# Optimization experiments

Measured on AMD Instinct MI355X. Metric: run time of the kernel, lower is better.

Reference implementation:

```python
import jax, jax.numpy as jnp
import numpy as np

N, H, HD = 512, 8, 128          # n_nodes, n_heads, h feature dim
M0, M1 = 256, 256               # mlp_units
NORM_CONST = 1.0


def setup_inputs() -> dict:
    key = jax.random.key(0)
    ks = jax.random.split(key, 16)
    def w(k, i, o, scale=1.0):
        return jax.random.normal(k, (i, o), jnp.float32) * (scale / np.sqrt(i))
    F = HD + H * H               # h_concat dim = 128 + 64 = 192
    EIN = H + 2 * F              # edge MLP input dim = 8 + 384 = 392
    return {
        "x": jax.random.normal(ks[0], (N, H, 3), jnp.float32),
        "h": jax.random.normal(ks[1], (N, HD), jnp.float32),
        # phi_e: MLP([256,256], silu, activate_final=True)
        "We0": w(ks[2], EIN, M0), "be0": jnp.zeros((M0,), jnp.float32),
        "We1": w(ks[3], M0, M1), "be1": jnp.zeros((M1,), jnp.float32),
        # phi_inf: Linear(1) + sigmoid
        "Winf": w(ks[4], M1, 1), "binf": jnp.zeros((1,), jnp.float32),
        # phi_x: MLP([256,256], silu, activate_final=True) -> Linear(n_heads) (variance-scaled small init)
        "Wx0": w(ks[5], M1, M0), "bx0": jnp.zeros((M0,), jnp.float32),
        "Wx1": w(ks[6], M0, M1), "bx1": jnp.zeros((M1,), jnp.float32),
        "Wxo": w(ks[7], M1, H, scale=0.03), "bxo": jnp.zeros((H,), jnp.float32),
        # phi_h: MLP([256,256], silu, activate_final=False)... note haiku MLP applies
        # activation between layers; final Linear(h_dim) appended in forward.
        "Wh0": w(ks[8], M1 + HD, M0), "bh0": jnp.zeros((M0,), jnp.float32),
        "Wh1": w(ks[9], M0, M1), "bh1": jnp.zeros((M1,), jnp.float32),
        "Who": w(ks[10], M1, HD), "bho": jnp.zeros((HD,), jnp.float32),
    }


def _forward(x, h, We0, be0, We1, be1, Winf, binf, Wx0, bx0, Wx1, bx1,
             Wxo, bxo, Wh0, bh0, Wh1, bh1, Who, bho):
    n, nh = x.shape[0], x.shape[1]
    silu = jax.nn.silu
    off = 1.0 - jnp.eye(n, dtype=x.dtype)                  # off-diagonal node mask
    # per-node head-pair squared distances -> [N, H*H] (diag naturally 0)
    dh = x[:, :, None, :] - x[:, None, :, :]               # [N,H,H,3]
    sqh = jnp.sum(dh * dh, axis=-1).reshape(n, nh * nh)
    hc = jnp.concatenate([h, sqh], axis=-1)                # [N, F]
    # all-pairs node diffs per head: dn[i,j,h] = x[j,h] - x[i,h]
    dn = x[None] - x[:, None]                              # [N,N,H,3]
    sqn = jnp.sum(dn * dn, axis=-1)                        # [N,N,H]
    F = hc.shape[-1]
    hc_j = jnp.broadcast_to(hc[None], (n, n, F))           # receiver-side: hc[j]
    hc_i = jnp.broadcast_to(hc[:, None], (n, n, F))        # sender-side: hc[i]
    edge_in = jnp.concatenate([sqn, hc_j, hc_i], axis=-1)  # [N,N,H+2F]
    # phi_e (activate_final=True), zero self-edges
    m = silu(silu(edge_in @ We0 + be0) @ We1 + be1) * off[:, :, None]
    # gate + message aggregation
    e = jax.nn.sigmoid(m @ Winf + binf)[..., 0] * off      # [N,N]
    m_i = jnp.einsum('ijd,ij->id', m, e)                   # [N,M1]
    # phi_x multi-head coordinate weights (tanh=False), zero self-edges
    px = (silu(silu(m @ Wx0 + bx0) @ Wx1 + bx1) @ Wxo + bxo) * off[:, :, None]
    # normalize_by_x_norm=True path
    norm = jnp.sqrt(sqn + 1e-8) + NORM_CONST               # [N,N,H]
    ndiff = (dn / norm[..., None]) * off[:, :, None, None]
    shift = jnp.einsum('ijhd,ijh->ihd', ndiff, px) / (n - 1)  # agg='mean'
    x_new = x + shift
    # phi_h with residual
    ph_in = jnp.concatenate([m_i, h], axis=-1)
    h_new = h + silu(silu(ph_in @ Wh0 + bh0) @ Wh1 + bh1) @ Who + bho
    return x_new, h_new


def reference(x, h, We0, be0, We1, be1, Winf, binf, Wx0, bx0, Wx1, bx1,
              Wxo, bxo, Wh0, bh0, Wh1, bh1, Who, bho):
    return _forward(x, h, We0, be0, We1, be1, Winf, binf, Wx0, bx0, Wx1, bx1,
                    Wxo, bxo, Wh0, bh0, Wh1, bh1, Who, bho)
```

## Files before the change

kernel.cpp:

```cpp
#include <hip/hip_runtime.h>
#include <math.h>

#define N_NODES 512
#define NH 8
#define HD 128
#define M 256
#define PITCH 264
#define JTILE 64
#define RPW 16

typedef __bf16 v8bf __attribute__((ext_vector_type(8)));
typedef float f32x4 __attribute__((ext_vector_type(4)));
typedef unsigned short us4v __attribute__((ext_vector_type(4)));

__device__ __forceinline__ float silu_f(float v) {
  return v * __builtin_amdgcn_rcpf(1.f + __expf(-v));
}
__device__ __forceinline__ float sigmoid_f(float v) {
  return __builtin_amdgcn_rcpf(1.f + __expf(-v));
}
__device__ __forceinline__ unsigned short f2bf(float f) {
  unsigned u = __float_as_uint(f);
  u += 0x7fffu + ((u >> 16) & 1u);
  return (unsigned short)(u >> 16);
}
__device__ __forceinline__ unsigned short f2bf_hi(float f) {
  return (unsigned short)((__float_as_uint(f) + 0x8000u) >> 16);
}
__device__ __forceinline__ float bf2f(unsigned short s) {
  return __uint_as_float(((unsigned)s) << 16);
}

__device__ __forceinline__ void gl2lds16(const unsigned short* g, unsigned short* l) {
  __builtin_amdgcn_global_load_lds(
      (const __attribute__((address_space(1))) unsigned int*)g,
      (__attribute__((address_space(3))) unsigned int*)l, 16, 0, 0);
}

__global__ __launch_bounds__(256) void k_pre(
    const float* __restrict__ x, const float* __restrict__ h,
    const float* __restrict__ We0, const float* __restrict__ be0,
    const float* __restrict__ We1, const float* __restrict__ Wx0,
    const float* __restrict__ Wx1, const float* __restrict__ Wxo,
    unsigned short* __restrict__ wsB,
    float* __restrict__ P, float* __restrict__ Q,
    float* __restrict__ mi, float* __restrict__ shift)
{
  const int t = threadIdx.x;
  if (blockIdx.x < 816) {
    const int gid = blockIdx.x * 256 + t;
    if (gid >= 208896) return;
    float val;
    if (gid < 196608) {
      const int layer = gid >> 16;
      const int i2 = gid & 65535;
      const int j = i2 & 7, lane = (i2 >> 3) & 63, nt = (i2 >> 9) & 15, kt = i2 >> 13;
      const int k = kt * 32 + (lane >> 4) * 8 + j;
      const int n = nt * 16 + (lane & 15);
      const float* W = (layer == 0) ? We1 : (layer == 1) ? Wx0 : Wx1;
      val = W[k * 256 + n];
    } else if (gid < 200704) {
      const int i2 = gid - 196608;
      const int j = i2 & 7, lane = (i2 >> 3) & 63, kt = (i2 >> 9) & 7;
      const int k = kt * 32 + (lane >> 4) * 8 + j;
      const int n = lane & 15;
      val = (n < 8) ? Wxo[k * 8 + n] : 0.f;
    } else {
      const int i2 = gid - 200704;
      const int j = i2 & 7, lane = (i2 >> 3) & 63, nt = i2 >> 9;
      const int quad = lane >> 4, lnib = lane & 15;
      val = (quad == 0) ? We0[j * 256 + nt * 16 + lnib] : 0.f;
    }
    wsB[gid] = f2bf(val);
    return;
  }
  const int i = blockIdx.x - 816;
  __shared__ float s_x[24];
  __shared__ float s_hc[192];
  mi[i * M + t] = 0.f;
  if (t < 24) { shift[i * 24 + t] = 0.f; s_x[t] = x[i * 24 + t]; }
  __syncthreads();
  if (t < HD) {
    s_hc[t] = h[i * HD + t];
  } else if (t < 192) {
    const int p = t - HD, a = p >> 3, b = p & 7;
    float s = 0.f;
#pragma unroll
    for (int d = 0; d < 3; ++d) {
      const float dx = s_x[a * 3 + d] - s_x[b * 3 + d];
      s = fmaf(dx, dx, s);
    }
    s_hc[t] = s;
  }
  __syncthreads();
  float p = 0.f, q = 0.f;
  for (int k = 0; k < 192; ++k) {
    const float hv = s_hc[k];
    p = fmaf(hv, We0[(8 + k) * M + t], p);
    q = fmaf(hv, We0[(200 + k) * M + t], q);
  }
  P[i * M + t] = p;
  Q[i * M + t] = q + be0[t];
}

__global__ __launch_bounds__(512, 4) void k_edge(
    const float* __restrict__ x,
    const float* __restrict__ P, const float* __restrict__ Q,
    const float* __restrict__ be1,
    const float* __restrict__ Winf, const float* __restrict__ binf,
    const float* __restrict__ bx0, const float* __restrict__ bx1,
    const float* __restrict__ bxo,
    const unsigned short* __restrict__ wsB,
    float* __restrict__ mi_acc, float* __restrict__ shift_acc)
{
  const int i  = blockIdx.x;
  const int j0 = blockIdx.y * JTILE;
  const int t  = threadIdx.x;
  const int lane = t & 63, wave = t >> 6;
  const int lnib = lane & 15, quad = lane >> 4;
  const int rg = wave >> 1, c = wave & 1;
  const int r0 = rg * RPW;
  const int jw = j0 + r0;
  const int cb = c * 128;

  __shared__ __align__(16) unsigned short a_act[JTILE * PITCH];
  __shared__ __align__(16) unsigned short B_buf[8192];
  __shared__ __align__(16) float s_sqn[JTILE][8];
  __shared__ __align__(16) unsigned short s_sqnb[JTILE][8];
  __shared__ float s_red[JTILE][2];
  __shared__ float s_e[JTILE];

  auto stage = [&](const unsigned short* __restrict__ Bg, int kt) {
    const unsigned short* src = Bg + kt * 8192 + wave * 1024 + lane * 8;
    unsigned short* dst = &B_buf[wave * 1024];
    gl2lds16(src,       dst);
    gl2lds16(src + 512, dst + 512);
  };

#pragma unroll
  for (int kk = 0; kk < 2; ++kk) {
    const int idx = kk * 64 + lane;
    const int r = idx >> 3, hh = idx & 7;
    const int j = jw + r;
    float s = 0.f;
#pragma unroll
    for (int d = 0; d < 3; ++d) {
      const float dx = x[j * 24 + hh * 3 + d] - x[i * 24 + hh * 3 + d];
      s = fmaf(dx, dx, s);
    }
    s_sqn[r0 + r][hh] = s;
    s_sqnb[r0 + r][hh] = f2bf(s);
  }

  const float binf0 = binf[0];

  f32x4 acc[8];

  {
#pragma unroll
    for (int nt = 0; nt < 8; ++nt)
#pragma unroll
      for (int reg = 0; reg < 4; ++reg)
        acc[nt][reg] = P[(jw + quad * 4 + reg) * M + cb + nt * 16 + lnib];
    const v8bf aS = *(const v8bf*)&s_sqnb[r0 + lnib][0];
    const unsigned short* B0 = wsB + 200704;
#pragma unroll
    for (int nt = 0; nt < 8; ++nt) {
      const v8bf bv = *(const v8bf*)&B0[((c * 8 + nt) * 64 + lane) * 8];
      acc[nt] = __builtin_amdgcn_mfma_f32_16x16x32_bf16(aS, bv, acc[nt], 0, 0, 0);
    }
#pragma unroll
    for (int nt = 0; nt < 8; ++nt) {
      const float qv = Q[i * M + cb + nt * 16 + lnib];
#pragma unroll
      for (int reg = 0; reg < 4; ++reg) {
        const int row = r0 + quad * 4 + reg;
        a_act[row * PITCH + cb + nt * 16 + lnib] = f2bf_hi(silu_f(acc[nt][reg] + qv));
      }
    }
  }

  auto run_gemm = [&](const unsigned short* __restrict__ Bg) {
#pragma unroll
    for (int kt = 0; kt < 8; ++kt) {
      __syncthreads();
      stage(Bg, kt);
      __syncthreads();
      const v8bf a0 = *(const v8bf*)&a_act[(r0 + lnib) * PITCH + kt * 32 + quad * 8];
#pragma unroll
      for (int nt = 0; nt < 8; ++nt) {
        const v8bf bv = *(const v8bf*)&B_buf[(c * 8 + nt) * 512 + lane * 8];
        acc[nt] = __builtin_amdgcn_mfma_f32_16x16x32_bf16(a0, bv, acc[nt], 0, 0, 0);
      }
    }
    __syncthreads();
  };

#pragma unroll
  for (int nt = 0; nt < 8; ++nt) {
    const float b = be1[cb + nt * 16 + lnib];
    acc[nt] = (f32x4){b, b, b, b};
  }
  run_gemm(wsB);
  {
    float ge[4] = {0.f, 0.f, 0.f, 0.f};
#pragma unroll
    for (int nt = 0; nt < 8; ++nt) {
      const float wfv = Winf[cb + nt * 16 + lnib];
#pragma unroll
      for (int reg = 0; reg < 4; ++reg) {
        float v = silu_f(acc[nt][reg]);
        const int row = r0 + quad * 4 + reg;
        if (j0 + row == i) v = 0.f;
        a_act[row * PITCH + cb + nt * 16 + lnib] = f2bf_hi(v);
        ge[reg] = fmaf(v, wfv, ge[reg]);
      }
    }
#pragma unroll
    for (int reg = 0; reg < 4; ++reg) {
      float g = ge[reg];
      g += __shfl_xor(g, 1);
      g += __shfl_xor(g, 2);
      g += __shfl_xor(g, 4);
      g += __shfl_xor(g, 8);
      if (lnib == 0) s_red[r0 + quad * 4 + reg][c] = g;
    }
  }
  __syncthreads();
  if (t < JTILE) s_e[t] = sigmoid_f(s_red[t][0] + s_red[t][1] + binf0);
  __syncthreads();

  {
    const int ch = cb + lane * 2;
    float m0 = 0.f, m1 = 0.f;
#pragma unroll
    for (int r = 0; r < RPW; ++r) {
      const unsigned mv = *(const unsigned*)&a_act[(r0 + r) * PITCH + ch];
      const float ev = s_e[r0 + r];
      m0 = fmaf(bf2f((unsigned short)(mv & 0xffffu)), ev, m0);
      m1 = fmaf(bf2f((unsigned short)(mv >> 16)), ev, m1);
    }
    atomicAdd(&mi_acc[i * M + ch + 0], m0);
    atomicAdd(&mi_acc[i * M + ch + 1], m1);
  }

#pragma unroll
  for (int nt = 0; nt < 8; ++nt) {
    const float b = bx0[cb + nt * 16 + lnib];
    acc[nt] = (f32x4){b, b, b, b};
  }
  run_gemm(wsB + 65536);
#pragma unroll
  for (int nt = 0; nt < 8; ++nt)
#pragma unroll
    for (int reg = 0; reg < 4; ++reg) {
      const int row = r0 + quad * 4 + reg;
      a_act[row * PITCH + cb + nt * 16 + lnib] = f2bf_hi(silu_f(acc[nt][reg]));
    }

#pragma unroll
  for (int nt = 0; nt < 8; ++nt) {
    const float b = bx1[cb + nt * 16 + lnib];
    acc[nt] = (f32x4){b, b, b, b};
  }
  run_gemm(wsB + 131072);
#pragma unroll
  for (int nt = 0; nt < 8; ++nt)
#pragma unroll
    for (int reg = 0; reg < 4; ++reg) {
      const int row = r0 + quad * 4 + reg;
      a_act[row * PITCH + cb + nt * 16 + lnib] = f2bf_hi(silu_f(acc[nt][reg]));
    }
  __syncthreads();

  if (c == 0) {
    f32x4 px;
    {
      const float b = (lnib < 8) ? bxo[lnib] : 0.f;
      px = (f32x4){b, b, b, b};
      const unsigned short* B = wsB + 196608;
#pragma unroll
      for (int kt = 0; kt < 8; ++kt) {
        const v8bf a0 = *(const v8bf*)&a_act[(r0 + lnib) * PITCH + kt * 32 + quad * 8];
        const v8bf bv = *(const v8bf*)&B[(kt * 64 + lane) * 8];
        px = __builtin_amdgcn_mfma_f32_16x16x32_bf16(a0, bv, px, 0, 0, 0);
      }
    }
    const int hh = lnib & 7;
    const float xi0 = x[i * 24 + hh * 3 + 0];
    const float xi1 = x[i * 24 + hh * 3 + 1];
    const float xi2 = x[i * 24 + hh * 3 + 2];
    float p0 = 0.f, p1 = 0.f, p2 = 0.f;
#pragma unroll
    for (int reg = 0; reg < 4; ++reg) {
      const int row = r0 + quad * 4 + reg;
      const int jg = j0 + row;
      if (jg != i) {
        const float pxv = px[reg];
        const float sq  = s_sqn[row][hh];
        const float f   = pxv * __builtin_amdgcn_rcpf(sqrtf(sq + 1e-8f) + 1.f);
        p0 = fmaf(x[jg * 24 + hh * 3 + 0] - xi0, f, p0);
        p1 = fmaf(x[jg * 24 + hh * 3 + 1] - xi1, f, p1);
        p2 = fmaf(x[jg * 24 + hh * 3 + 2] - xi2, f, p2);
      }
    }
    p0 += __shfl_xor(p0, 16); p0 += __shfl_xor(p0, 32);
    p1 += __shfl_xor(p1, 16); p1 += __shfl_xor(p1, 32);
    p2 += __shfl_xor(p2, 16); p2 += __shfl_xor(p2, 32);
    if (lane < 8) {
      atomicAdd(&shift_acc[i * 24 + hh * 3 + 0], p0);
      atomicAdd(&shift_acc[i * 24 + hh * 3 + 1], p1);
      atomicAdd(&shift_acc[i * 24 + hh * 3 + 2], p2);
    }
  }
}

__global__ __launch_bounds__(256) void k_hout(
    const float* __restrict__ x, const float* __restrict__ shift,
    const float* __restrict__ h, const float* __restrict__ mi,
    const float* __restrict__ Wh0, const float* __restrict__ bh0,
    const float* __restrict__ Wh1, const float* __restrict__ bh1,
    const float* __restrict__ Who, const float* __restrict__ bho,
    float* __restrict__ out_x, float* __restrict__ out_h)
{
  const int i = blockIdx.x, t = threadIdx.x;
  __shared__ float s_in[M + HD];
  __shared__ float s_b[M];
  if (t < 24) out_x[i * 24 + t] = x[i * 24 + t] + shift[i * 24 + t] * (1.f / 511.f);
  s_in[t] = mi[i * M + t];
  if (t < HD) s_in[M + t] = h[i * HD + t];
  __syncthreads();
  float acc = bh0[t];
  for (int k = 0; k < M + HD; ++k) acc = fmaf(s_in[k], Wh0[k * M + t], acc);
  s_b[t] = silu_f(acc);
  __syncthreads();
  float acc2 = bh1[t];
  for (int k = 0; k < M; ++k) acc2 = fmaf(s_b[k], Wh1[k * M + t], acc2);
  const float a1v = silu_f(acc2);
  __syncthreads();
  s_in[t] = a1v;
  __syncthreads();
  if (t < HD) {
    float o = bho[t];
    for (int k = 0; k < M; ++k) o = fmaf(s_in[k], Who[k * HD + t], o);
    out_h[i * HD + t] = h[i * HD + t] + o;
  }
}

extern "C" void kernel_launch(void* const* d_in, const int* in_sizes, int n_in,
                              void* d_out, int out_size, void* d_ws, size_t ws_size,
                              hipStream_t stream)
{
  const float* x    = (const float*)d_in[0];
  const float* h    = (const float*)d_in[1];
  const float* We0  = (const float*)d_in[2];
  const float* be0  = (const float*)d_in[3];
  const float* We1  = (const float*)d_in[4];
  const float* be1  = (const float*)d_in[5];
  const float* Winf = (const float*)d_in[6];
  const float* binf = (const float*)d_in[7];
  const float* Wx0  = (const float*)d_in[8];
  const float* bx0  = (const float*)d_in[9];
  const float* Wx1  = (const float*)d_in[10];
  const float* bx1  = (const float*)d_in[11];
  const float* Wxo  = (const float*)d_in[12];
  const float* bxo  = (const float*)d_in[13];
  const float* Wh0  = (const float*)d_in[14];
  const float* bh0  = (const float*)d_in[15];
  const float* Wh1  = (const float*)d_in[16];
  const float* bh1  = (const float*)d_in[17];
  const float* Who  = (const float*)d_in[18];
  const float* bho  = (const float*)d_in[19];

  float* out_x = (float*)d_out;
  float* out_h = out_x + N_NODES * NH * 3;

  float* ws    = (float*)d_ws;
  float* mi    = ws;
  float* shift = ws + 131072;
  float* P     = ws + 143360;
  float* Q     = ws + 274432;
  unsigned short* wsB = (unsigned short*)(ws + 405504);

  k_pre<<<816 + N_NODES, 256, 0, stream>>>(
      x, h, We0, be0, We1, Wx0, Wx1, Wxo, wsB, P, Q, mi, shift);
  k_edge<<<dim3(N_NODES, N_NODES / JTILE), 512, 0, stream>>>(
      x, P, Q, be1, Winf, binf, bx0, bx1, bxo, wsB, mi, shift);
  k_hout<<<N_NODES, 256, 0, stream>>>(
      x, shift, h, mi, Wh0, bh0, Wh1, bh1, Who, bho, out_x, out_h);
}
```

Measured before the change: 321.6 us.

## Double-buffer weight staging in LDS and coalesce weight repack reads

The edge kernel's GEMM loop now double-buffers the bf16 weight tiles in LDS. The next k-tile, or the first tile of the next layer's GEMM, is prefetched while MFMAs run on the current tile, which cuts one of the two barriers per k-step. The pre-kernel weight repack now reads the fp32 weights in source order (coalesced) and scatters the writes into the swizzled layout. In exchange the LDS footprint grows by 16 KB per block, which may lower occupancy, and the async-copy completion now depends on the single per-iteration barrier.

```diff
diff --git a/kernel.cpp b/kernel.cpp
--- a/kernel.cpp
+++ b/kernel.cpp
@@ -51,27 +51,40 @@
     const int gid = blockIdx.x * 256 + t;
     if (gid >= 208896) return;
     float val;
+    int dst;
     if (gid < 196608) {
-      const int layer = gid >> 16;
-      const int i2 = gid & 65535;
-      const int j = i2 & 7, lane = (i2 >> 3) & 63, nt = (i2 >> 9) & 15, kt = i2 >> 13;
-      const int k = kt * 32 + (lane >> 4) * 8 + j;
-      const int n = nt * 16 + (lane & 15);
+      const int layer = gid >> 16, e = gid & 65535;
+      const int k = e >> 8, n = e & 255;
       const float* W = (layer == 0) ? We1 : (layer == 1) ? Wx0 : Wx1;
-      val = W[k * 256 + n];
+      val = W[e];
+      const int kt = k >> 5, w = k & 31, quad = w >> 3, j = w & 7;
+      const int nt = n >> 4, lnib = n & 15;
+      dst = layer * 65536 + ((kt * 16 + nt) * 64 + quad * 16 + lnib) * 8 + j;
+    } else if (gid < 198656) {
+      const int e = gid - 196608;
+      val = Wxo[e];
+      const int k = e >> 3, col = e & 7;
+      const int kt = k >> 5, w = k & 31, quad = w >> 3, j = w & 7;
+      dst = 196608 + (kt * 64 + quad * 16 + col) * 8 + j;
     } else if (gid < 200704) {
-      const int i2 = gid - 196608;
-      const int j = i2 & 7, lane = (i2 >> 3) & 63, kt = (i2 >> 9) & 7;
-      const int k = kt * 32 + (lane >> 4) * 8 + j;
-      const int n = lane & 15;
-      val = (n < 8) ? Wxo[k * 8 + n] : 0.f;
+      const int e = gid - 198656;
+      val = 0.f;
+      const int k = e >> 3, col = e & 7;
+      const int kt = k >> 5, w = k & 31, quad = w >> 3, j = w & 7;
+      dst = 196608 + (kt * 64 + quad * 16 + col + 8) * 8 + j;
+    } else if (gid < 202752) {
+      const int e = gid - 200704;
+      val = We0[e];
+      const int j = e >> 8, n = e & 255, nt = n >> 4, lnib = n & 15;
+      dst = 200704 + (nt * 64 + lnib) * 8 + j;
     } else {
-      const int i2 = gid - 200704;
-      const int j = i2 & 7, lane = (i2 >> 3) & 63, nt = i2 >> 9;
-      const int quad = lane >> 4, lnib = lane & 15;
-      val = (quad == 0) ? We0[j * 256 + nt * 16 + lnib] : 0.f;
-    }
-    wsB[gid] = f2bf(val);
+      const int e = gid - 202752;
+      val = 0.f;
+      const int q = 1 + (e >> 11), rem = e & 2047;
+      const int j = rem & 7, lnib = (rem >> 3) & 15, nt = rem >> 7;
+      dst = 200704 + (nt * 64 + q * 16 + lnib) * 8 + j;
+    }
+    wsB[dst] = f2bf(val);
     return;
   }
   const int i = blockIdx.x - 816;
@@ -124,15 +137,15 @@
   const int cb = c * 128;
 
   __shared__ __align__(16) unsigned short a_act[JTILE * PITCH];
-  __shared__ __align__(16) unsigned short B_buf[8192];
+  __shared__ __align__(16) unsigned short B_buf[2][8192];
   __shared__ __align__(16) float s_sqn[JTILE][8];
   __shared__ __align__(16) unsigned short s_sqnb[JTILE][8];
   __shared__ float s_red[JTILE][2];
   __shared__ float s_e[JTILE];
 
-  auto stage = [&](const unsigned short* __restrict__ Bg, int kt) {
+  auto stage = [&](const unsigned short* __restrict__ Bg, int kt, int which) {
     const unsigned short* src = Bg + kt * 8192 + wave * 1024 + lane * 8;
-    unsigned short* dst = &B_buf[wave * 1024];
+    unsigned short* dst = &B_buf[which][wave * 1024];
     gl2lds16(src,       dst);
     gl2lds16(src + 512, dst + 512);
   };
@@ -152,6 +165,8 @@
     s_sqnb[r0 + r][hh] = f2bf(s);
   }
 
+  stage(wsB, 0, 0);
+
   const float binf0 = binf[0];
 
   f32x4 acc[8];
@@ -180,20 +195,21 @@
     }
   }
 
-  auto run_gemm = [&](const unsigned short* __restrict__ Bg) {
+  auto run_gemm = [&](const unsigned short* __restrict__ Bg,
+                      const unsigned short* __restrict__ Bnext) {
+    __syncthreads();
 #pragma unroll
     for (int kt = 0; kt < 8; ++kt) {
-      __syncthreads();
-      stage(Bg, kt);
-      __syncthreads();
+      if (kt < 7)      stage(Bg, kt + 1, (kt + 1) & 1);
+      else if (Bnext)  stage(Bnext, 0, 0);
       const v8bf a0 = *(const v8bf*)&a_act[(r0 + lnib) * PITCH + kt * 32 + quad * 8];
 #pragma unroll
       for (int nt = 0; nt < 8; ++nt) {
-        const v8bf bv = *(const v8bf*)&B_buf[(c * 8 + nt) * 512 + lane * 8];
+        const v8bf bv = *(const v8bf*)&B_buf[kt & 1][(c * 8 + nt) * 512 + lane * 8];
         acc[nt] = __builtin_amdgcn_mfma_f32_16x16x32_bf16(a0, bv, acc[nt], 0, 0, 0);
       }
-    }
-    __syncthreads();
+      __syncthreads();
+    }
   };
 
 #pragma unroll
@@ -201,7 +217,7 @@
     const float b = be1[cb + nt * 16 + lnib];
     acc[nt] = (f32x4){b, b, b, b};
   }
-  run_gemm(wsB);
+  run_gemm(wsB, wsB + 65536);
   {
     float ge[4] = {0.f, 0.f, 0.f, 0.f};
 #pragma unroll
@@ -249,7 +265,7 @@
     const float b = bx0[cb + nt * 16 + lnib];
     acc[nt] = (f32x4){b, b, b, b};
   }
-  run_gemm(wsB + 65536);
+  run_gemm(wsB + 65536, wsB + 131072);
 #pragma unroll
   for (int nt = 0; nt < 8; ++nt)
 #pragma unroll
@@ -263,7 +279,7 @@
     const float b = bx1[cb + nt * 16 + lnib];
     acc[nt] = (f32x4){b, b, b, b};
   }
-  run_gemm(wsB + 131072);
+  run_gemm(wsB + 131072, nullptr);
 #pragma unroll
   for (int nt = 0; nt < 8; ++nt)
 #pragma unroll
```

Measured after the change: 306.5 us, median of 2. -4.7%, faster.
